# Optimization experiments

Measured on AMD Instinct MI355X. Metric: run time of the kernel, lower is better.

## Reference

```python
import jax, jax.numpy as jnp
import numpy as np

B, D, H, C = 512, 1024, 512, 4


def setup_inputs() -> dict:
    key = jax.random.key(0)
    k_x, k_v, k_w = jax.random.split(key, 3)
    # x holds categorical values in [0, C) used as float multipliers
    x = jax.random.randint(k_x, (B, D), 0, C).astype(jnp.float32)
    # xavier_normal_ per torch fan computation: V fan_in=D*C, fan_out=H*C; W fan_in=D, fan_out=H
    V = jax.random.normal(k_v, (H, D, C), jnp.float32) * np.float32(np.sqrt(2.0 / (D * C + H * C)))
    b = jnp.zeros((D, C), jnp.float32)
    W = jax.random.normal(k_w, (H, D), jnp.float32) * np.float32(np.sqrt(2.0 / (D + H)))
    c = jnp.zeros((1, H), jnp.float32)
    return {"x": x, "V": V, "b": b, "W": W, "c": c}


def _nade_forward(x, V, b, W, c):
    Bsz = x.shape[0]
    a0 = jnp.broadcast_to(c, (Bsz, c.shape[1]))  # [B, H]
    # per-step slices stacked along leading D axis for lax.scan
    xs = (jnp.transpose(V, (1, 0, 2)),  # [D, H, C]
          b,                            # [D, C]
          W.T,                          # [D, H]
          x.T)                          # [D, B]

    def step(a, inp):
        V_d, b_d, w_d, x_d = inp
        h = jax.nn.sigmoid(a)                 # [B, H]
        logits = h @ V_d + b_d                # [B, C]
        p = jax.nn.log_softmax(logits, axis=1)
        a_new = a + x_d[:, None] * w_d[None, :]  # rank-1 update of running preactivation
        return a_new, (logits, p)

    _, (logits, p) = jax.lax.scan(step, a0, xs)   # each [D, B, C]
    y_hat = jnp.transpose(logits, (1, 0, 2)).reshape(Bsz, -1)  # [B, D*C], d-major blocks of size C
    p_hat = jnp.transpose(p, (1, 0, 2)).reshape(Bsz, -1)
    return y_hat, p_hat


def reference(x, V, b, W, c):
    return _nade_forward(x, V, b, W, c)
```

## Files before the change

### kernel.cpp

```cpp
#include <hip/hip_runtime.h>
#include <hip/hip_fp16.h>


#define Bv 512
#define Dv 1024
#define Hv 512
#define Cv 4
#define Kv 64
#define DCv 16

#define L2E 1.4426950408889634f
#define LN2 0.6931471805599453f

typedef __attribute__((ext_vector_type(8))) short short8;
typedef __attribute__((ext_vector_type(4))) float f32x4;
typedef __attribute__((ext_vector_type(2))) float v2f;

__device__ __forceinline__ float fexp2(float x) { return __builtin_amdgcn_exp2f(x); }
__device__ __forceinline__ float flog2(float x) { return __builtin_amdgcn_logf(x); }
__device__ __forceinline__ float frcp(float x)  { return __builtin_amdgcn_rcpf(x); }

__device__ __forceinline__ v2f fma2(v2f a, v2f b, v2f c) {
#if __has_builtin(__builtin_elementwise_fma)
    return __builtin_elementwise_fma(a, b, c);
#else
    v2f r; r.x = fmaf(a.x, b.x, c.x); r.y = fmaf(a.y, b.y, c.y); return r;
#endif
}

__device__ __forceinline__ float sig1t(float a) {
    float e = fexp2(-a);
    float q = 1.0f + e;
    float r0 = __int_as_float(0x7EF311C3 - __float_as_int(q));
    float t = fmaf(-q, r0, 2.0f);
    return r0 * t;
}

__device__ __forceinline__ unsigned bf16pk(float lo, float hi) {
    return __builtin_amdgcn_perm(__float_as_uint(hi), __float_as_uint(lo), 0x07060302u);
}
__device__ __forceinline__ unsigned short bf16rne(float f) {
    unsigned u = __float_as_uint(f);
    return (unsigned short)((u + 0x7FFFu + ((u >> 16) & 1u)) >> 16);
}

__global__ __launch_bounds__(512) void k_prep(
        const float* __restrict__ V, const float* __restrict__ W,
        const float* __restrict__ x, unsigned short* __restrict__ VtA4,
        float* __restrict__ WtL, float* __restrict__ xt,
        __half* __restrict__ P) {
    __shared__ char smem[17408];
    const int bid = blockIdx.x;
    if (bid < 256) {
        unsigned short* tile = (unsigned short*)smem;
        const int d0 = bid * 4;
        const int dd = threadIdx.x & 3;
        const int hb0 = threadIdx.x >> 2;
#pragma unroll
        for (int p = 0; p < 4; ++p) {
            int h = p * 128 + hb0;
            float4 v = *(const float4*)(V + ((size_t)h * Dv + d0 + dd) * Cv);
            int hb = h >> 5, q = (h >> 3) & 3, j = h & 7;
            int base = ((dd * 16 + hb) * 16 + q * 4) * 8 + j;
            tile[base + 0]  = bf16rne(v.x);
            tile[base + 8]  = bf16rne(v.y);
            tile[base + 16] = bf16rne(v.z);
            tile[base + 24] = bf16rne(v.w);
        }
        __syncthreads();
        uint4* dst = (uint4*)(VtA4 + (size_t)d0 * 2048);
        const uint4* src = (const uint4*)tile;
#pragma unroll
        for (int p = 0; p < 2; ++p)
            dst[p * 512 + threadIdx.x] = src[p * 512 + threadIdx.x];
    } else if (bid < 512) {
        float (*t)[65] = (float (*)[65])smem;
        const int mb   = (bid - 256) >> 7;
        const int tile = (bid - 256) & 127;
        const int tr   = tile >> 4;
        const int tc   = tile & 15;
        const float* src = mb ? x : W;
        float* dst       = mb ? xt : WtL;
        const float scale = mb ? 1.0f : L2E;
        const int lx = threadIdx.x & 15;
        const int ly = threadIdx.x >> 4;
#pragma unroll
        for (int r = 0; r < 64; r += 32) {
            int row = r + ly;
            float4 v = *(const float4*)(src + (size_t)(tr * 64 + row) * Dv + tc * 64 + lx * 4);
            t[row][lx * 4 + 0] = v.x;
            t[row][lx * 4 + 1] = v.y;
            t[row][lx * 4 + 2] = v.z;
            t[row][lx * 4 + 3] = v.w;
        }
        __syncthreads();
#pragma unroll
        for (int r = 0; r < 64; r += 32) {
            int row = r + ly;
            float4 o = make_float4(t[lx * 4 + 0][row] * scale,
                                   t[lx * 4 + 1][row] * scale,
                                   t[lx * 4 + 2][row] * scale,
                                   t[lx * 4 + 3][row] * scale);
            *(float4*)(dst + (size_t)(tc * 64 + row) * 512 + tr * 64 + lx * 4) = o;
        }
    } else {
        float* xs = (float*)smem;
        const int pb = bid - 512;
        const int k  = pb >> 6;
        const int bg = pb & 63;
        const int h  = threadIdx.x;
        const int d0 = k * DCv;
        if (threadIdx.x < DCv * 8) {
            int g = threadIdx.x & 7;
            int j = threadIdx.x >> 3;
            xs[j * 8 + g] = x[(size_t)(bg * 8 + g) * Dv + d0 + j];
        }
        __syncthreads();

        float wr[DCv];
        const float* wp = W + (size_t)h * Dv + d0;
#pragma unroll
        for (int j4 = 0; j4 < DCv; j4 += 4)
            *(float4*)(wr + j4) = *(const float4*)(wp + j4);

        float acc[8];
#pragma unroll
        for (int g = 0; g < 8; ++g) acc[g] = 0.0f;
#pragma unroll
        for (int j = 0; j < DCv; ++j) {
            float wv = wr[j];
            const float4 x0 = *(const float4*)(xs + j * 8);
            const float4 x1 = *(const float4*)(xs + j * 8 + 4);
            acc[0] = fmaf(x0.x, wv, acc[0]);
            acc[1] = fmaf(x0.y, wv, acc[1]);
            acc[2] = fmaf(x0.z, wv, acc[2]);
            acc[3] = fmaf(x0.w, wv, acc[3]);
            acc[4] = fmaf(x1.x, wv, acc[4]);
            acc[5] = fmaf(x1.y, wv, acc[5]);
            acc[6] = fmaf(x1.z, wv, acc[6]);
            acc[7] = fmaf(x1.w, wv, acc[7]);
        }
#pragma unroll
        for (int g = 0; g < 8; ++g)
            P[((size_t)k * Bv + bg * 8 + g) * Hv + h] = __float2half(acc[g] * L2E);
    }
}

__global__ void k_prefix(__half* __restrict__ A0, const float* __restrict__ cbias) {
    int gid = blockIdx.x * blockDim.x + threadIdx.x;
    int h = gid & (Hv - 1);
    int bi = gid >> 9;
    float run = cbias[h] * L2E;
    __half* p = A0 + (size_t)bi * Hv + h;
#pragma unroll 4
    for (int k = 0; k < Kv; ++k) {
        float t = __half2float(p[(size_t)k * Bv * Hv]);
        p[(size_t)k * Bv * Hv] = __float2half(run);
        run += t;
    }
}

__global__ __launch_bounds__(128) void k_main(
        const float* __restrict__ xt, const float* __restrict__ bbias,
        const unsigned short* __restrict__ VtA4, const float* __restrict__ WtL,
        const __half* __restrict__ A0, float* __restrict__ out) {
    const int k    = blockIdx.x >> 5;
    const int bg   = blockIdx.x & 31;
    const int wv   = threadIdx.x >> 6;
    const int lane = threadIdx.x & 63;
    const int bl   = lane & 15;
    const int quad = lane >> 4;
    const int b    = bg * 16 + bl;
    const int d0   = k * DCv;

    __shared__ f32x4 red[2][2][2][64];

    v2f a2[32];
    {
        const __half* ap = A0 + ((size_t)k * Bv + b) * Hv + wv * 256 + quad * 8;
#pragma unroll
        for (int kb = 0; kb < 8; ++kb) {
            union { uint4 u; __half2 h2[4]; } t;
            t.u = *(const uint4*)(ap + kb * 32);
#pragma unroll
            for (int tt = 0; tt < 4; ++tt) {
                float2 f = __half22float2(t.h2[tt]);
                a2[kb * 4 + tt] = (v2f){f.x, f.y};
            }
        }
    }

    const int blc = (bl < 4) ? bl : 0;
    const unsigned short* vp = VtA4 + (((size_t)d0 * 16 + wv * 8) * 16 + quad * 4 + blc) * 8;
    const float* wp = WtL + (size_t)d0 * Hv + wv * 256 + quad * 8;
    const float* xp = xt + (size_t)d0 * Bv + b;
    const float* bp = bbias + (d0 + wv) * Cv;
    float* sy = out + (size_t)b * Dv * Cv + (d0 + wv) * Cv;
    float* spp = sy + (size_t)Bv * Dv * Cv;

    for (int i1 = 0; i1 < DCv / 2; ++i1) {
        float xdA = xp[0];
        float xdB = xp[Bv];
        float4 bbv = *(const float4*)bp;

        f32x4 acc0 = {0.f, 0.f, 0.f, 0.f};
        f32x4 acc1 = {0.f, 0.f, 0.f, 0.f};
#pragma unroll
        for (int kb = 0; kb < 8; ++kb) {
            union { unsigned u[4]; short8 s; } cv;
#pragma unroll
            for (int t = 0; t < 4; ++t) {
                v2f aa = a2[kb * 4 + t];
                cv.u[t] = bf16pk(sig1t(aa.x), sig1t(aa.y));
            }
            short8 af = *(const short8*)(vp + kb * 128);
            if (kb & 1)
                acc1 = __builtin_amdgcn_mfma_f32_16x16x32_bf16(af, cv.s, acc1, 0, 0, 0);
            else
                acc0 = __builtin_amdgcn_mfma_f32_16x16x32_bf16(af, cv.s, acc0, 0, 0, 0);
        }
        f32x4 accA = acc0 + acc1;
        v2f xA2 = {xdA, xdA};
#pragma unroll
        for (int kb = 0; kb < 8; ++kb) {
            float4 w0 = *(const float4*)(wp + kb * 32);
            float4 w1 = *(const float4*)(wp + kb * 32 + 4);
            a2[kb*4+0] = fma2(xA2, (v2f){w0.x, w0.y}, a2[kb*4+0]);
            a2[kb*4+1] = fma2(xA2, (v2f){w0.z, w0.w}, a2[kb*4+1]);
            a2[kb*4+2] = fma2(xA2, (v2f){w1.x, w1.y}, a2[kb*4+2]);
            a2[kb*4+3] = fma2(xA2, (v2f){w1.z, w1.w}, a2[kb*4+3]);
        }

        f32x4 acc2 = {0.f, 0.f, 0.f, 0.f};
        f32x4 acc3 = {0.f, 0.f, 0.f, 0.f};
#pragma unroll
        for (int kb = 0; kb < 8; ++kb) {
            union { unsigned u[4]; short8 s; } cv;
#pragma unroll
            for (int t = 0; t < 4; ++t) {
                v2f aa = a2[kb * 4 + t];
                cv.u[t] = bf16pk(sig1t(aa.x), sig1t(aa.y));
            }
            short8 af = *(const short8*)(vp + 2048 + kb * 128);
            if (kb & 1)
                acc3 = __builtin_amdgcn_mfma_f32_16x16x32_bf16(af, cv.s, acc3, 0, 0, 0);
            else
                acc2 = __builtin_amdgcn_mfma_f32_16x16x32_bf16(af, cv.s, acc2, 0, 0, 0);
        }
        f32x4 accB = acc2 + acc3;
        v2f xB2 = {xdB, xdB};
#pragma unroll
        for (int kb = 0; kb < 8; ++kb) {
            float4 w0 = *(const float4*)(wp + Hv + kb * 32);
            float4 w1 = *(const float4*)(wp + Hv + kb * 32 + 4);
            a2[kb*4+0] = fma2(xB2, (v2f){w0.x, w0.y}, a2[kb*4+0]);
            a2[kb*4+1] = fma2(xB2, (v2f){w0.z, w0.w}, a2[kb*4+1]);
            a2[kb*4+2] = fma2(xB2, (v2f){w1.x, w1.y}, a2[kb*4+2]);
            a2[kb*4+3] = fma2(xB2, (v2f){w1.z, w1.w}, a2[kb*4+3]);
        }

        red[i1 & 1][0][wv][lane] = accA;
        red[i1 & 1][1][wv][lane] = accB;
        __syncthreads();

        f32x4 s = red[i1 & 1][wv][0][lane] + red[i1 & 1][wv][1][lane];
        float w0 = s.x + bbv.x;
        float w1 = s.y + bbv.y;
        float w2 = s.z + bbv.z;
        float w3 = s.w + bbv.w;
        float mx = fmaxf(fmaxf(w0, w1), fmaxf(w2, w3));
        float e0 = fexp2((w0 - mx) * L2E);
        float e1 = fexp2((w1 - mx) * L2E);
        float e2 = fexp2((w2 - mx) * L2E);
        float e3 = fexp2((w3 - mx) * L2E);
        float lse = mx + flog2(e0 + e1 + e2 + e3) * LN2;
        if (quad == 0) {
            *(float4*)sy  = make_float4(w0, w1, w2, w3);
            *(float4*)spp = make_float4(w0 - lse, w1 - lse, w2 - lse, w3 - lse);
        }

        vp += 2 * 2048;
        wp += 2 * Hv;
        xp += 2 * Bv;
        bp += 2 * Cv;
        sy += 2 * Cv;
        spp += 2 * Cv;
    }
}

extern "C" void kernel_launch(void* const* d_in, const int* in_sizes, int n_in,
                              void* d_out, int out_size, void* d_ws, size_t ws_size,
                              hipStream_t stream) {
    const float* x  = (const float*)d_in[0];
    const float* V  = (const float*)d_in[1];
    const float* bb = (const float*)d_in[2];
    const float* W  = (const float*)d_in[3];
    const float* cb = (const float*)d_in[4];
    float* out = (float*)d_out;

    char* ws = (char*)d_ws;
    unsigned short* VtA4 = (unsigned short*)ws;
    float* WtL = (float*)(ws + (size_t)4 * 1024 * 1024);
    float* xt  = (float*)(ws + (size_t)6 * 1024 * 1024);
    __half* A0 = (__half*)(ws + (size_t)8 * 1024 * 1024);

    k_prep<<<512 + Kv * (Bv / 8), 512, 0, stream>>>(V, W, x, VtA4, WtL, xt, A0);
    k_prefix<<<(Bv * Hv) / 256, 256, 0, stream>>>(A0, cb);
    k_main<<<Kv * 32, 128, 0, stream>>>(xt, bb, VtA4, WtL, A0, out);
}
```

Before: 186.7 us.

## Fuse prep, prefix and main into one cooperative kernel with grid syncs

Merges the three launches into a single cooperative kernel of 1024 blocks of 128 threads, separated by grid-wide syncs, to remove launch gaps between stages. Doubles the chunk length (DCv 32, Kv 32), which halves the prefix length and the parallel chunk count but lengthens each block's serial loop. Also replaces the bit-trick Newton reciprocal in the sigmoid with the hardware rcp. The cooperative launch requires every block to be resident at once, and the longer per-block serial chain cuts parallelism in the main stage.

```diff
diff --git a/kernel.cpp b/kernel.cpp
--- a/kernel.cpp
+++ b/kernel.cpp
@@ -1,13 +1,16 @@
 #include <hip/hip_runtime.h>
 #include <hip/hip_fp16.h>
-
+#include <hip/hip_cooperative_groups.h>
+
+
+namespace cg = cooperative_groups;
 
 #define Bv 512
 #define Dv 1024
 #define Hv 512
 #define Cv 4
-#define Kv 64
-#define DCv 16
+#define Kv 32
+#define DCv 32
 
 #define L2E 1.4426950408889634f
 #define LN2 0.6931471805599453f
@@ -28,14 +31,6 @@
 #endif
 }
 
-__device__ __forceinline__ float sig1t(float a) {
-    float e = fexp2(-a);
-    float q = 1.0f + e;
-    float r0 = __int_as_float(0x7EF311C3 - __float_as_int(q));
-    float t = fmaf(-q, r0, 2.0f);
-    return r0 * t;
-}
-
 __device__ __forceinline__ unsigned bf16pk(float lo, float hi) {
     return __builtin_amdgcn_perm(__float_as_uint(hi), __float_as_uint(lo), 0x07060302u);
 }
@@ -44,21 +39,26 @@
     return (unsigned short)((u + 0x7FFFu + ((u >> 16) & 1u)) >> 16);
 }
 
-__global__ __launch_bounds__(512) void k_prep(
-        const float* __restrict__ V, const float* __restrict__ W,
-        const float* __restrict__ x, unsigned short* __restrict__ VtA4,
-        float* __restrict__ WtL, float* __restrict__ xt,
-        __half* __restrict__ P) {
-    __shared__ char smem[17408];
+__global__ __launch_bounds__(128, 4) void k_all(
+        const float* __restrict__ x, const float* __restrict__ V,
+        const float* __restrict__ bbias, const float* __restrict__ W,
+        const float* __restrict__ cb,
+        unsigned short* __restrict__ VtA4, float* __restrict__ WtL,
+        float* __restrict__ xt, __half* __restrict__ A0,
+        float* __restrict__ out) {
+    __shared__ __align__(16) char smem[16384];
     const int bid = blockIdx.x;
+    const int tid = threadIdx.x;
+    cg::grid_group grid = cg::this_grid();
+
     if (bid < 256) {
         unsigned short* tile = (unsigned short*)smem;
         const int d0 = bid * 4;
-        const int dd = threadIdx.x & 3;
-        const int hb0 = threadIdx.x >> 2;
-#pragma unroll
-        for (int p = 0; p < 4; ++p) {
-            int h = p * 128 + hb0;
+#pragma unroll
+        for (int p = 0; p < 16; ++p) {
+            int idx = p * 128 + tid;
+            int dd = idx & 3;
+            int h  = idx >> 2;
             float4 v = *(const float4*)(V + ((size_t)h * Dv + d0 + dd) * Cv);
             int hb = h >> 5, q = (h >> 3) & 3, j = h & 7;
             int base = ((dd * 16 + hb) * 16 + q * 4) * 8 + j;
@@ -71,220 +71,241 @@
         uint4* dst = (uint4*)(VtA4 + (size_t)d0 * 2048);
         const uint4* src = (const uint4*)tile;
 #pragma unroll
-        for (int p = 0; p < 2; ++p)
-            dst[p * 512 + threadIdx.x] = src[p * 512 + threadIdx.x];
-    } else if (bid < 512) {
-        float (*t)[65] = (float (*)[65])smem;
-        const int mb   = (bid - 256) >> 7;
-        const int tile = (bid - 256) & 127;
-        const int tr   = tile >> 4;
-        const int tc   = tile & 15;
+        for (int p = 0; p < 8; ++p)
+            dst[p * 128 + tid] = src[p * 128 + tid];
+    } else if (bid < 768) {
+        float (*td)[33] = (float (*)[33])smem;
+        const int idx0 = bid - 256;
+        const int mb   = idx0 >> 8;
+        const int tile = idx0 & 255;
+        const int tr   = tile >> 5;
+        const int tc   = tile & 31;
         const float* src = mb ? x : W;
         float* dst       = mb ? xt : WtL;
         const float scale = mb ? 1.0f : L2E;
-        const int lx = threadIdx.x & 15;
-        const int ly = threadIdx.x >> 4;
-#pragma unroll
-        for (int r = 0; r < 64; r += 32) {
-            int row = r + ly;
-            float4 v = *(const float4*)(src + (size_t)(tr * 64 + row) * Dv + tc * 64 + lx * 4);
-            t[row][lx * 4 + 0] = v.x;
-            t[row][lx * 4 + 1] = v.y;
-            t[row][lx * 4 + 2] = v.z;
-            t[row][lx * 4 + 3] = v.w;
+#pragma unroll
+        for (int p = 0; p < 4; ++p) {
+            int idx = p * 128 + tid;
+            int c4  = idx & 7;
+            int row = idx >> 3;
+            float4 v = *(const float4*)(src + (size_t)(tr * 64 + row) * Dv + tc * 32 + c4 * 4);
+            td[row][c4 * 4 + 0] = v.x;
+            td[row][c4 * 4 + 1] = v.y;
+            td[row][c4 * 4 + 2] = v.z;
+            td[row][c4 * 4 + 3] = v.w;
         }
         __syncthreads();
 #pragma unroll
-        for (int r = 0; r < 64; r += 32) {
-            int row = r + ly;
-            float4 o = make_float4(t[lx * 4 + 0][row] * scale,
-                                   t[lx * 4 + 1][row] * scale,
-                                   t[lx * 4 + 2][row] * scale,
-                                   t[lx * 4 + 3][row] * scale);
-            *(float4*)(dst + (size_t)(tc * 64 + row) * 512 + tr * 64 + lx * 4) = o;
+        for (int p = 0; p < 4; ++p) {
+            int idx  = p * 128 + tid;
+            int dc4  = idx & 15;
+            int drow = idx >> 4;
+            float4 o = make_float4(td[dc4 * 4 + 0][drow] * scale,
+                                   td[dc4 * 4 + 1][drow] * scale,
+                                   td[dc4 * 4 + 2][drow] * scale,
+                                   td[dc4 * 4 + 3][drow] * scale);
+            *(float4*)(dst + (size_t)(tc * 32 + drow) * Hv + tr * 64 + dc4 * 4) = o;
         }
     } else {
         float* xs = (float*)smem;
-        const int pb = bid - 512;
-        const int k  = pb >> 6;
-        const int bg = pb & 63;
-        const int h  = threadIdx.x;
-        const int d0 = k * DCv;
-        if (threadIdx.x < DCv * 8) {
-            int g = threadIdx.x & 7;
-            int j = threadIdx.x >> 3;
-            xs[j * 8 + g] = x[(size_t)(bg * 8 + g) * Dv + d0 + j];
+        const int pbi = bid - 768;
+        const int k   = pbi >> 3;
+        const int bg0 = (pbi & 7) * 64;
+        const int d0  = k * DCv;
+#pragma unroll
+        for (int p = 0; p < 4; ++p) {
+            int idx = p * 128 + tid;
+            int q4 = idx & 7;
+            int g  = idx >> 3;
+            float4 v = *(const float4*)(x + (size_t)(bg0 + g) * Dv + d0 + q4 * 4);
+            xs[(q4 * 4 + 0) * 68 + g] = v.x;
+            xs[(q4 * 4 + 1) * 68 + g] = v.y;
+            xs[(q4 * 4 + 2) * 68 + g] = v.z;
+            xs[(q4 * 4 + 3) * 68 + g] = v.w;
         }
         __syncthreads();
-
-        float wr[DCv];
-        const float* wp = W + (size_t)h * Dv + d0;
-#pragma unroll
-        for (int j4 = 0; j4 < DCv; j4 += 4)
-            *(float4*)(wr + j4) = *(const float4*)(wp + j4);
-
-        float acc[8];
-#pragma unroll
-        for (int g = 0; g < 8; ++g) acc[g] = 0.0f;
-#pragma unroll
-        for (int j = 0; j < DCv; ++j) {
-            float wv = wr[j];
-            const float4 x0 = *(const float4*)(xs + j * 8);
-            const float4 x1 = *(const float4*)(xs + j * 8 + 4);
-            acc[0] = fmaf(x0.x, wv, acc[0]);
-            acc[1] = fmaf(x0.y, wv, acc[1]);
-            acc[2] = fmaf(x0.z, wv, acc[2]);
-            acc[3] = fmaf(x0.w, wv, acc[3]);
-            acc[4] = fmaf(x1.x, wv, acc[4]);
-            acc[5] = fmaf(x1.y, wv, acc[5]);
-            acc[6] = fmaf(x1.z, wv, acc[6]);
-            acc[7] = fmaf(x1.w, wv, acc[7]);
-        }
-#pragma unroll
-        for (int g = 0; g < 8; ++g)
-            P[((size_t)k * Bv + bg * 8 + g) * Hv + h] = __float2half(acc[g] * L2E);
+#pragma unroll
+        for (int hx = 0; hx < 4; ++hx) {
+            const int h = tid + hx * 128;
+            float wr[DCv];
+            const float* wp = W + (size_t)h * Dv + d0;
+#pragma unroll
+            for (int j4 = 0; j4 < DCv; j4 += 4)
+                *(float4*)(wr + j4) = *(const float4*)(wp + j4);
+#pragma unroll
+            for (int u = 0; u < 8; ++u) {
+                float acc[8];
+#pragma unroll
+                for (int g = 0; g < 8; ++g) acc[g] = 0.0f;
+#pragma unroll
+                for (int j = 0; j < DCv; ++j) {
+                    float wv = wr[j];
+                    const float4 xa = *(const float4*)(xs + j * 68 + u * 8);
+                    const float4 xb = *(const float4*)(xs + j * 68 + u * 8 + 4);
+                    acc[0] = fmaf(xa.x, wv, acc[0]);
+                    acc[1] = fmaf(xa.y, wv, acc[1]);
+                    acc[2] = fmaf(xa.z, wv, acc[2]);
+                    acc[3] = fmaf(xa.w, wv, acc[3]);
+                    acc[4] = fmaf(xb.x, wv, acc[4]);
+                    acc[5] = fmaf(xb.y, wv, acc[5]);
+                    acc[6] = fmaf(xb.z, wv, acc[6]);
+                    acc[7] = fmaf(xb.w, wv, acc[7]);
+                }
+#pragma unroll
+                for (int g = 0; g < 8; ++g)
+                    A0[((size_t)k * Bv + bg0 + u * 8 + g) * Hv + h] =
+                        __float2half(acc[g] * L2E);
+            }
+        }
     }
-}
-
-__global__ void k_prefix(__half* __restrict__ A0, const float* __restrict__ cbias) {
-    int gid = blockIdx.x * blockDim.x + threadIdx.x;
-    int h = gid & (Hv - 1);
-    int bi = gid >> 9;
-    float run = cbias[h] * L2E;
-    __half* p = A0 + (size_t)bi * Hv + h;
+
+    grid.sync();
+
+    {
+#pragma unroll
+        for (int it = 0; it < 2; ++it) {
+            int gid = it * 131072 + bid * 128 + tid;
+            int h = gid & (Hv - 1);
+            int b = gid >> 9;
+            float run = cb[h] * L2E;
+            __half* p = A0 + (size_t)b * Hv + h;
 #pragma unroll 4
-    for (int k = 0; k < Kv; ++k) {
-        float t = __half2float(p[(size_t)k * Bv * Hv]);
-        p[(size_t)k * Bv * Hv] = __float2half(run);
-        run += t;
+            for (int k = 0; k < Kv; ++k) {
+                float t = __half2float(p[(size_t)k * Bv * Hv]);
+                p[(size_t)k * Bv * Hv] = __float2half(run);
+                run += t;
+            }
+        }
     }
-}
-
-__global__ __launch_bounds__(128) void k_main(
-        const float* __restrict__ xt, const float* __restrict__ bbias,
-        const unsigned short* __restrict__ VtA4, const float* __restrict__ WtL,
-        const __half* __restrict__ A0, float* __restrict__ out) {
-    const int k    = blockIdx.x >> 5;
-    const int bg   = blockIdx.x & 31;
-    const int wv   = threadIdx.x >> 6;
-    const int lane = threadIdx.x & 63;
-    const int bl   = lane & 15;
-    const int quad = lane >> 4;
-    const int b    = bg * 16 + bl;
-    const int d0   = k * DCv;
-
-    __shared__ f32x4 red[2][2][2][64];
-
-    v2f a2[32];
+
+    grid.sync();
+
     {
-        const __half* ap = A0 + ((size_t)k * Bv + b) * Hv + wv * 256 + quad * 8;
-#pragma unroll
-        for (int kb = 0; kb < 8; ++kb) {
-            union { uint4 u; __half2 h2[4]; } t;
-            t.u = *(const uint4*)(ap + kb * 32);
-#pragma unroll
-            for (int tt = 0; tt < 4; ++tt) {
-                float2 f = __half22float2(t.h2[tt]);
-                a2[kb * 4 + tt] = (v2f){f.x, f.y};
-            }
-        }
-    }
-
-    const int blc = (bl < 4) ? bl : 0;
-    const unsigned short* vp = VtA4 + (((size_t)d0 * 16 + wv * 8) * 16 + quad * 4 + blc) * 8;
-    const float* wp = WtL + (size_t)d0 * Hv + wv * 256 + quad * 8;
-    const float* xp = xt + (size_t)d0 * Bv + b;
-    const float* bp = bbias + (d0 + wv) * Cv;
-    float* sy = out + (size_t)b * Dv * Cv + (d0 + wv) * Cv;
-    float* spp = sy + (size_t)Bv * Dv * Cv;
-
-    for (int i1 = 0; i1 < DCv / 2; ++i1) {
-        float xdA = xp[0];
-        float xdB = xp[Bv];
-        float4 bbv = *(const float4*)bp;
-
-        f32x4 acc0 = {0.f, 0.f, 0.f, 0.f};
-        f32x4 acc1 = {0.f, 0.f, 0.f, 0.f};
-#pragma unroll
-        for (int kb = 0; kb < 8; ++kb) {
-            union { unsigned u[4]; short8 s; } cv;
-#pragma unroll
-            for (int t = 0; t < 4; ++t) {
-                v2f aa = a2[kb * 4 + t];
-                cv.u[t] = bf16pk(sig1t(aa.x), sig1t(aa.y));
-            }
-            short8 af = *(const short8*)(vp + kb * 128);
-            if (kb & 1)
-                acc1 = __builtin_amdgcn_mfma_f32_16x16x32_bf16(af, cv.s, acc1, 0, 0, 0);
-            else
-                acc0 = __builtin_amdgcn_mfma_f32_16x16x32_bf16(af, cv.s, acc0, 0, 0, 0);
-        }
-        f32x4 accA = acc0 + acc1;
-        v2f xA2 = {xdA, xdA};
-#pragma unroll
-        for (int kb = 0; kb < 8; ++kb) {
-            float4 w0 = *(const float4*)(wp + kb * 32);
-            float4 w1 = *(const float4*)(wp + kb * 32 + 4);
-            a2[kb*4+0] = fma2(xA2, (v2f){w0.x, w0.y}, a2[kb*4+0]);
-            a2[kb*4+1] = fma2(xA2, (v2f){w0.z, w0.w}, a2[kb*4+1]);
-            a2[kb*4+2] = fma2(xA2, (v2f){w1.x, w1.y}, a2[kb*4+2]);
-            a2[kb*4+3] = fma2(xA2, (v2f){w1.z, w1.w}, a2[kb*4+3]);
-        }
-
-        f32x4 acc2 = {0.f, 0.f, 0.f, 0.f};
-        f32x4 acc3 = {0.f, 0.f, 0.f, 0.f};
-#pragma unroll
-        for (int kb = 0; kb < 8; ++kb) {
-            union { unsigned u[4]; short8 s; } cv;
-#pragma unroll
-            for (int t = 0; t < 4; ++t) {
-                v2f aa = a2[kb * 4 + t];
-                cv.u[t] = bf16pk(sig1t(aa.x), sig1t(aa.y));
-            }
-            short8 af = *(const short8*)(vp + 2048 + kb * 128);
-            if (kb & 1)
-                acc3 = __builtin_amdgcn_mfma_f32_16x16x32_bf16(af, cv.s, acc3, 0, 0, 0);
-            else
-                acc2 = __builtin_amdgcn_mfma_f32_16x16x32_bf16(af, cv.s, acc2, 0, 0, 0);
-        }
-        f32x4 accB = acc2 + acc3;
-        v2f xB2 = {xdB, xdB};
-#pragma unroll
-        for (int kb = 0; kb < 8; ++kb) {
-            float4 w0 = *(const float4*)(wp + Hv + kb * 32);
-            float4 w1 = *(const float4*)(wp + Hv + kb * 32 + 4);
-            a2[kb*4+0] = fma2(xB2, (v2f){w0.x, w0.y}, a2[kb*4+0]);
-            a2[kb*4+1] = fma2(xB2, (v2f){w0.z, w0.w}, a2[kb*4+1]);
-            a2[kb*4+2] = fma2(xB2, (v2f){w1.x, w1.y}, a2[kb*4+2]);
-            a2[kb*4+3] = fma2(xB2, (v2f){w1.z, w1.w}, a2[kb*4+3]);
-        }
-
-        red[i1 & 1][0][wv][lane] = accA;
-        red[i1 & 1][1][wv][lane] = accB;
-        __syncthreads();
-
-        f32x4 s = red[i1 & 1][wv][0][lane] + red[i1 & 1][wv][1][lane];
-        float w0 = s.x + bbv.x;
-        float w1 = s.y + bbv.y;
-        float w2 = s.z + bbv.z;
-        float w3 = s.w + bbv.w;
-        float mx = fmaxf(fmaxf(w0, w1), fmaxf(w2, w3));
-        float e0 = fexp2((w0 - mx) * L2E);
-        float e1 = fexp2((w1 - mx) * L2E);
-        float e2 = fexp2((w2 - mx) * L2E);
-        float e3 = fexp2((w3 - mx) * L2E);
-        float lse = mx + flog2(e0 + e1 + e2 + e3) * LN2;
-        if (quad == 0) {
-            *(float4*)sy  = make_float4(w0, w1, w2, w3);
-            *(float4*)spp = make_float4(w0 - lse, w1 - lse, w2 - lse, w3 - lse);
-        }
-
-        vp += 2 * 2048;
-        wp += 2 * Hv;
-        xp += 2 * Bv;
-        bp += 2 * Cv;
-        sy += 2 * Cv;
-        spp += 2 * Cv;
+        f32x4 (*red)[2][2][64] = (f32x4 (*)[2][2][64])smem;
+        const int k    = bid >> 5;
+        const int bg   = bid & 31;
+        const int wv   = tid >> 6;
+        const int lane = tid & 63;
+        const int bl   = lane & 15;
+        const int quad = lane >> 4;
+        const int b    = bg * 16 + bl;
+        const int d0   = k * DCv;
+
+        v2f a2[32];
+        {
+            const __half* ap = A0 + ((size_t)k * Bv + b) * Hv + wv * 256 + quad * 8;
+#pragma unroll
+            for (int kb = 0; kb < 8; ++kb) {
+                union { uint4 u; __half2 h2[4]; } t;
+                t.u = *(const uint4*)(ap + kb * 32);
+#pragma unroll
+                for (int tt = 0; tt < 4; ++tt) {
+                    float2 f = __half22float2(t.h2[tt]);
+                    a2[kb * 4 + tt] = (v2f){f.x, f.y};
+                }
+            }
+        }
+
+        const int blc = (bl < 4) ? bl : 0;
+        const unsigned short* vp = VtA4 + (((size_t)d0 * 16 + wv * 8) * 16 + quad * 4 + blc) * 8;
+        const float* wp = WtL + (size_t)d0 * Hv + wv * 256 + quad * 8;
+        const float* xp = xt + (size_t)d0 * Bv + b;
+        const float* bp = bbias + (d0 + wv) * Cv;
+        float* sy = out + (size_t)b * Dv * Cv + (d0 + wv) * Cv;
+        float* spp = sy + (size_t)Bv * Dv * Cv;
+
+        for (int i1 = 0; i1 < DCv / 2; ++i1) {
+            float xdA = xp[0];
+            float xdB = xp[Bv];
+            float4 bbv = *(const float4*)bp;
+
+            f32x4 acc0 = {0.f, 0.f, 0.f, 0.f};
+            f32x4 acc1 = {0.f, 0.f, 0.f, 0.f};
+#pragma unroll
+            for (int kb = 0; kb < 8; ++kb) {
+                union { unsigned u[4]; short8 s; } cv;
+#pragma unroll
+                for (int t = 0; t < 4; ++t) {
+                    v2f aa = a2[kb * 4 + t];
+                    float s0 = frcp(1.0f + fexp2(-aa.x));
+                    float s1 = frcp(1.0f + fexp2(-aa.y));
+                    cv.u[t] = bf16pk(s0, s1);
+                }
+                short8 af = *(const short8*)(vp + kb * 128);
+                if (kb & 1)
+                    acc1 = __builtin_amdgcn_mfma_f32_16x16x32_bf16(af, cv.s, acc1, 0, 0, 0);
+                else
+                    acc0 = __builtin_amdgcn_mfma_f32_16x16x32_bf16(af, cv.s, acc0, 0, 0, 0);
+            }
+            f32x4 accA = acc0 + acc1;
+            v2f xA2 = {xdA, xdA};
+#pragma unroll
+            for (int kb = 0; kb < 8; ++kb) {
+                float4 w0 = *(const float4*)(wp + kb * 32);
+                float4 w1 = *(const float4*)(wp + kb * 32 + 4);
+                a2[kb*4+0] = fma2(xA2, (v2f){w0.x, w0.y}, a2[kb*4+0]);
+                a2[kb*4+1] = fma2(xA2, (v2f){w0.z, w0.w}, a2[kb*4+1]);
+                a2[kb*4+2] = fma2(xA2, (v2f){w1.x, w1.y}, a2[kb*4+2]);
+                a2[kb*4+3] = fma2(xA2, (v2f){w1.z, w1.w}, a2[kb*4+3]);
+            }
+
+            f32x4 acc2 = {0.f, 0.f, 0.f, 0.f};
+            f32x4 acc3 = {0.f, 0.f, 0.f, 0.f};
+#pragma unroll
+            for (int kb = 0; kb < 8; ++kb) {
+                union { unsigned u[4]; short8 s; } cv;
+#pragma unroll
+                for (int t = 0; t < 4; ++t) {
+                    v2f aa = a2[kb * 4 + t];
+                    float s0 = frcp(1.0f + fexp2(-aa.x));
+                    float s1 = frcp(1.0f + fexp2(-aa.y));
+                    cv.u[t] = bf16pk(s0, s1);
+                }
+                short8 af = *(const short8*)(vp + 2048 + kb * 128);
+                if (kb & 1)
+                    acc3 = __builtin_amdgcn_mfma_f32_16x16x32_bf16(af, cv.s, acc3, 0, 0, 0);
+                else
+                    acc2 = __builtin_amdgcn_mfma_f32_16x16x32_bf16(af, cv.s, acc2, 0, 0, 0);
+            }
+            f32x4 accB = acc2 + acc3;
+            v2f xB2 = {xdB, xdB};
+#pragma unroll
+            for (int kb = 0; kb < 8; ++kb) {
+                float4 w0 = *(const float4*)(wp + Hv + kb * 32);
+                float4 w1 = *(const float4*)(wp + Hv + kb * 32 + 4);
+                a2[kb*4+0] = fma2(xB2, (v2f){w0.x, w0.y}, a2[kb*4+0]);
+                a2[kb*4+1] = fma2(xB2, (v2f){w0.z, w0.w}, a2[kb*4+1]);
+                a2[kb*4+2] = fma2(xB2, (v2f){w1.x, w1.y}, a2[kb*4+2]);
+                a2[kb*4+3] = fma2(xB2, (v2f){w1.z, w1.w}, a2[kb*4+3]);
+            }
+
+            red[i1 & 1][0][wv][lane] = accA;
+            red[i1 & 1][1][wv][lane] = accB;
+            __syncthreads();
+
+            f32x4 s = red[i1 & 1][wv][0][lane] + red[i1 & 1][wv][1][lane];
+            float w0 = s.x + bbv.x;
+            float w1 = s.y + bbv.y;
+            float w2 = s.z + bbv.z;
+            float w3 = s.w + bbv.w;
+            float mx = fmaxf(fmaxf(w0, w1), fmaxf(w2, w3));
+            float e0 = fexp2((w0 - mx) * L2E);
+            float e1 = fexp2((w1 - mx) * L2E);
+            float e2 = fexp2((w2 - mx) * L2E);
+            float e3 = fexp2((w3 - mx) * L2E);
+            float lse = mx + flog2(e0 + e1 + e2 + e3) * LN2;
+            if (quad == 0) {
+                *(float4*)sy  = make_float4(w0, w1, w2, w3);
+                *(float4*)spp = make_float4(w0 - lse, w1 - lse, w2 - lse, w3 - lse);
+            }
+
+            vp += 2 * 2048;
+            wp += 2 * Hv;
+            xp += 2 * Bv;
+            bp += 2 * Cv;
+            sy += 2 * Cv;
+            spp += 2 * Cv;
+        }
     }
 }
 
@@ -304,7 +325,8 @@
     float* xt  = (float*)(ws + (size_t)6 * 1024 * 1024);
     __half* A0 = (__half*)(ws + (size_t)8 * 1024 * 1024);
 
-    k_prep<<<512 + Kv * (Bv / 8), 512, 0, stream>>>(V, W, x, VtA4, WtL, xt, A0);
-    k_prefix<<<(Bv * Hv) / 256, 256, 0, stream>>>(A0, cb);
-    k_main<<<Kv * 32, 128, 0, stream>>>(xt, bb, VtA4, WtL, A0, out);
-}
+    void* args[] = {(void*)&x, (void*)&V, (void*)&bb, (void*)&W, (void*)&cb,
+                    (void*)&VtA4, (void*)&WtL, (void*)&xt, (void*)&A0, (void*)&out};
+    hipLaunchCooperativeKernel((const void*)k_all, dim3(Kv * 32), dim3(128),
+                               args, 0, stream);
+}
```

Measured after the change: 691.4 us. +270.3%, slower.
